# Kernel optimization log

Hardware: AMD Instinct MI355X
Metric: run time of the kernel (lower is better)

The kernel has to match this reference:

```python
import jax, jax.numpy as jnp
import numpy as np

CLAMP_MAX = float(np.log(100.0))  # temperature clamp from MoELayer


def setup_inputs() -> dict:
    key = jax.random.key(0)
    ks = jax.random.split(key, 4)
    N, D, H, E = 524288, 128, 512, 8
    x = jax.random.normal(ks[0], (N, D), dtype=jnp.float32)
    # per-expert MLP params, stacked along expert axis; scaled like torch Linear init
    W1 = jax.random.normal(ks[1], (E, D, H), dtype=jnp.float32) / np.sqrt(D)
    b1 = jnp.zeros((E, H), dtype=jnp.float32)
    W2 = jax.random.normal(ks[2], (E, H, D), dtype=jnp.float32) / np.sqrt(H)
    b2 = jnp.zeros((E, D), dtype=jnp.float32)
    temperature = jnp.full((1,), np.log(2.0), dtype=jnp.float32)  # init from MoELayer
    return {"x": x, "W1": W1, "b1": b1, "W2": W2, "b2": b2,
            "temperature": temperature}


def reference(x, W1, b1, W2, b2, temperature):
    # Pretraining proportional router: tokens split into E contiguous equal
    # chunks (route_prob == 1), so dispatch/combine is a reshape.
    E = W1.shape[0]
    N, D = x.shape
    xe = x.reshape(E, N // E, D)                      # [E, n, D] dispatched tokens
    h = jax.nn.relu(jnp.einsum('end,edh->enh', xe, W1) + b1[:, None, :])
    y = jnp.einsum('enh,ehd->end', h, W2) + b2[:, None, :]
    logit_scale = jnp.exp(jnp.minimum(temperature, CLAMP_MAX))  # scalar [1]
    out = y.reshape(N, D) * logit_scale
    return out
```

## Files before the change

kernel.cpp:

```cpp
#include <hip/hip_runtime.h>


#define CLAMP_MAXV 4.605170185988091f

typedef __attribute__((ext_vector_type(8))) short s16x8;
typedef __attribute__((ext_vector_type(4))) float f32x4;
typedef __attribute__((ext_vector_type(4))) unsigned short u16x4;
typedef __attribute__((ext_vector_type(8))) unsigned short u16x8;

static __device__ __forceinline__ unsigned short f2bf(float f) {
  union { float f; unsigned int u; } v; v.f = f;
  unsigned int r = v.u + 0x7FFFu + ((v.u >> 16) & 1u);
  return (unsigned short)(r >> 16);
}

static __device__ __forceinline__ void gll16(const void* src, void* dst) {
  __builtin_amdgcn_global_load_lds((const __attribute__((address_space(1))) void*)src,
                                   (__attribute__((address_space(3))) void*)dst, 16, 0, 0);
}

#define LBAR() do { \
  asm volatile("s_waitcnt lgkmcnt(0)" ::: "memory"); \
  __builtin_amdgcn_s_barrier(); \
  __builtin_amdgcn_sched_barrier(0); \
} while (0)

__global__ void conv_w(const float* __restrict__ W1, const float* __restrict__ W2,
                       unsigned short* __restrict__ w1t, unsigned short* __restrict__ w2t) {
  int idx = blockIdx.x * 256 + threadIdx.x;
  if (idx < 65536) {
    int h  = idx & 511;
    int d0 = ((idx >> 9) & 15) << 3;
    int e  = idx >> 13;
    const float* src = W1 + ((size_t)e << 16);
    u16x8 v;
#pragma unroll
    for (int j = 0; j < 8; ++j) v[j] = f2bf(src[(size_t)(d0 + j) * 512 + h]);
    *(u16x8*)(w1t + ((((size_t)e << 9) + h) << 7) + d0) = v;
  } else {
    int i2 = idx - 65536;
    int d  = i2 & 127;
    int h0 = ((i2 >> 7) & 63) << 3;
    int e  = i2 >> 13;
    const float* src = W2 + ((size_t)e << 16);
    u16x8 v;
#pragma unroll
    for (int j = 0; j < 8; ++j) v[j] = f2bf(src[(size_t)(h0 + j) * 128 + d]);
    *(u16x8*)(w2t + ((((size_t)e << 7) + d) << 9) + h0) = v;
  }
}

__global__ __launch_bounds__(1024, 4) void moe_fused(
    const float* __restrict__ x,
    const float* __restrict__ b1,
    const float* __restrict__ b2,
    const float* __restrict__ temp,
    const unsigned short* __restrict__ w1t,
    const unsigned short* __restrict__ w2t,
    float* __restrict__ out)
{
  __shared__ __align__(16) char smem[133120];
  char* const w1s  = smem;
  char* const hsb0 = smem + 98304;
  char* const hsb1 = smem + 106496;
  char* const xs   = smem + 114688;
  float* const b1s = (float*)(smem + 131072);

  const int tid  = threadIdx.x;
  const int lane = tid & 63;
  const int wid  = tid >> 6;
  const int l15  = lane & 15;
  const int lg   = lane >> 4;
  const int blk  = blockIdx.x;
  const int e    = blk >> 6;
  const size_t tok0 = (size_t)blk << 10;

  const unsigned short* w1g = w1t + ((size_t)e << 16);
  const unsigned short* w2g = w2t + ((size_t)e << 16);
  const float* xblk = x + (tok0 << 7);
  float* const oblk = out + (tok0 << 7);

#pragma unroll
  for (int k = 0; k < 6; ++k) {
    int s = tid + (k << 10);
    int hl = s >> 4, sr = s & 15;
    gll16(w1g + ((size_t)(hl + 128) << 7) + ((sr ^ (hl & 7)) << 3), w1s + (s << 4));
  }

  if (tid < 512) b1s[tid] = b1[(e << 9) + tid];

  f32x4 xv[2];
  xv[0] = *(const f32x4*)(xblk + (tid << 3));
  xv[1] = *(const f32x4*)(xblk + (tid << 3) + 4);

  const int xtok = tid >> 4;
  const unsigned xaddr = (unsigned)((xtok << 8) + ((tid & 15) << 4)) ^ (unsigned)((xtok & 7) << 4);

  if (wid < 8) {
    const int hr  = wid & 3;
    const int tq0 = (wid >> 2) << 5;
    const unsigned hl2 = (unsigned)(((hr << 4) + (lg << 2)) << 1);

    s16x8 w1r[2][4];
#pragma unroll
    for (int c = 0; c < 2; ++c) {
      const int hrow = (c << 6) + (hr << 4) + l15;
#pragma unroll
      for (int ks = 0; ks < 4; ++ks)
        w1r[c][ks] = *(const s16x8*)(w1g + ((size_t)hrow << 7) + (ks << 5) + (lg << 3));
    }

    __syncthreads();

#pragma unroll 1
    for (int t = 0; t < 16; ++t) {
      u16x8 p;
#pragma unroll
      for (int i = 0; i < 8; ++i) p[i] = f2bf(xv[i >> 2][i & 3]);
      *(u16x8*)(xs + xaddr) = p;
      LBAR();

      s16x8 xb[2][4];
#pragma unroll
      for (int j = 0; j < 2; ++j) {
        int tk = tq0 + (j << 4) + l15;
#pragma unroll
        for (int ks = 0; ks < 4; ++ks) {
          unsigned koff = (unsigned)((ks << 6) + (lg << 4));
          xb[j][ks] = *(const s16x8*)(xs + (((unsigned)(tk << 8) + koff) ^ (unsigned)((tk & 7) << 4)));
        }
      }

#pragma unroll
      for (int c = 0; c <= 8; ++c) {
        if (c < 8) {
          f32x4 bias = *(const f32x4*)(b1s + (c << 6) + (hr << 4) + (lg << 2));
          f32x4 acc1[2];
          acc1[0] = (f32x4){0.f, 0.f, 0.f, 0.f};
          acc1[1] = (f32x4){0.f, 0.f, 0.f, 0.f};
          if (c < 2) {
#pragma unroll
            for (int j = 0; j < 2; ++j)
#pragma unroll
              for (int ks = 0; ks < 4; ++ks)
                acc1[j] = __builtin_amdgcn_mfma_f32_16x16x32_bf16(w1r[c][ks], xb[j][ks], acc1[j], 0, 0, 0);
          } else {
            const int hrow = (c << 6) + (hr << 4) + l15;
            const unsigned hswz = (unsigned)((hrow & 7) << 4);
            s16x8 a[4];
#pragma unroll
            for (int ks = 0; ks < 4; ++ks) {
              unsigned koff = (unsigned)((ks << 6) + (lg << 4));
              a[ks] = *(const s16x8*)(w1s + (((unsigned)((hrow - 128) << 8) + koff) ^ hswz));
            }
#pragma unroll
            for (int j = 0; j < 2; ++j)
#pragma unroll
              for (int ks = 0; ks < 4; ++ks)
                acc1[j] = __builtin_amdgcn_mfma_f32_16x16x32_bf16(a[ks], xb[j][ks], acc1[j], 0, 0, 0);
          }

          char* const hw = (c & 1) ? hsb1 : hsb0;
#pragma unroll
          for (int j = 0; j < 2; ++j) {
            int tk = tq0 + (j << 4) + l15;
            u16x4 qv;
#pragma unroll
            for (int r = 0; r < 4; ++r)
              qv[r] = f2bf(fmaxf(acc1[j][r] + bias[r], 0.f));
            *(u16x4*)(hw + (((unsigned)(tk << 7) + hl2) ^ (unsigned)((tk & 7) << 4))) = qv;
          }
        }
        if (c == 4 && t < 15) {
          const float* xn = xblk + (((size_t)t + 1) << 13);
          xv[0] = *(const f32x4*)(xn + (tid << 3));
          xv[1] = *(const f32x4*)(xn + (tid << 3) + 4);
        }
        LBAR();
      }
    }
  } else {
    const int cw = wid - 8;
    const int dlane = (cw << 4) + l15;

    s16x8 w2f[8][2];
#pragma unroll
    for (int c = 0; c < 8; ++c)
#pragma unroll
      for (int ks = 0; ks < 2; ++ks)
        w2f[c][ks] = *(const s16x8*)(w2g + ((size_t)dlane << 9) + (c << 6) + (ks << 5) + (lg << 3));

    const float b2v   = b2[(e << 7) + dlane];
    const float scale = expf(fminf(temp[0], CLAMP_MAXV));

    __syncthreads();

#pragma unroll 1
    for (int t = 0; t < 16; ++t) {
      u16x8 p;
#pragma unroll
      for (int i = 0; i < 8; ++i) p[i] = f2bf(xv[i >> 2][i & 3]);
      *(u16x8*)(xs + xaddr) = p;
      LBAR();

      f32x4 acc2[4];
#pragma unroll
      for (int i = 0; i < 4; ++i) acc2[i] = (f32x4){0.f, 0.f, 0.f, 0.f};

#pragma unroll
      for (int c = 0; c <= 8; ++c) {
        if (c >= 1) {
          const int cc = c - 1;
          char* const hrd = (cc & 1) ? hsb1 : hsb0;
#pragma unroll
          for (int ii = 0; ii < 4; ++ii) {
            int tk = (ii << 4) + l15;
            unsigned tswz = (unsigned)((tk & 7) << 4);
#pragma unroll
            for (int ks = 0; ks < 2; ++ks) {
              unsigned koff = (unsigned)((ks << 6) + (lg << 4));
              s16x8 ha = *(const s16x8*)(hrd + (((unsigned)(tk << 7) + koff) ^ tswz));
              acc2[ii] = __builtin_amdgcn_mfma_f32_16x16x32_bf16(ha, w2f[cc][ks], acc2[ii], 0, 0, 0);
            }
          }
        }
        if (c == 4 && t < 15) {
          const float* xn = xblk + (((size_t)t + 1) << 13);
          xv[0] = *(const f32x4*)(xn + (tid << 3));
          xv[1] = *(const f32x4*)(xn + (tid << 3) + 4);
        }
        LBAR();
      }

      float* og = oblk + ((size_t)t << 13);
#pragma unroll
      for (int i = 0; i < 4; ++i) {
#pragma unroll
        for (int r = 0; r < 4; ++r) {
          int tk = (i << 4) + (lg << 2) + r;
          og[((size_t)tk << 7) + dlane] = (acc2[i][r] + b2v) * scale;
        }
      }
    }
  }
}

__global__ void moe_naive(const float* __restrict__ x, const float* __restrict__ W1,
                          const float* __restrict__ b1, const float* __restrict__ W2,
                          const float* __restrict__ b2, const float* __restrict__ temp,
                          float* __restrict__ out) {
  __shared__ float xr[128];
  __shared__ float hrow[512];
  int t = blockIdx.x;
  int e = t >> 16;
  int tx = threadIdx.x;
  xr[tx] = x[((size_t)t << 7) + tx];
  __syncthreads();
  const float* w1e = W1 + ((size_t)e << 16);
  for (int h = tx; h < 512; h += 128) {
    float s = b1[(e << 9) + h];
    for (int d = 0; d < 128; ++d) s += xr[d] * w1e[(size_t)d * 512 + h];
    hrow[h] = fmaxf(s, 0.f);
  }
  __syncthreads();
  const float* w2e = W2 + ((size_t)e << 16);
  float s = b2[(e << 7) + tx];
  for (int h = 0; h < 512; ++h) s += hrow[h] * w2e[(size_t)h * 128 + tx];
  out[((size_t)t << 7) + tx] = s * expf(fminf(temp[0], CLAMP_MAXV));
}

extern "C" void kernel_launch(void* const* d_in, const int* in_sizes, int n_in,
                              void* d_out, int out_size, void* d_ws, size_t ws_size,
                              hipStream_t stream) {
  const float* x    = (const float*)d_in[0];
  const float* W1   = (const float*)d_in[1];
  const float* b1   = (const float*)d_in[2];
  const float* W2   = (const float*)d_in[3];
  const float* b2   = (const float*)d_in[4];
  const float* temp = (const float*)d_in[5];
  float* out = (float*)d_out;

  const size_t WS_NEEDED = 2u * 524288u * sizeof(unsigned short);
  if (ws_size >= WS_NEEDED) {
    unsigned short* w1t = (unsigned short*)d_ws;
    unsigned short* w2t = w1t + 524288;
    conv_w<<<512, 256, 0, stream>>>(W1, W2, w1t, w2t);
    moe_fused<<<512, 1024, 0, stream>>>(x, b1, b2, temp, w1t, w2t, out);
  } else {
    moe_naive<<<524288, 128, 0, stream>>>(x, W1, b1, W2, b2, temp, out);
  }
}
```

Measured before the change: 178.6 us.

## Software-pipeline MoE stages across token tiles to drop per-tile barriers

Restructures the warp-specialized loop so the final W2 chunk of each tile and its output store run in the first step of the next tile. This removes the extra ninth barrier step per tile. The x tile conversion to bf16 and the xb register reloads are moved inside the chunk loop, hiding them behind MFMA work instead of paying for them in a separate barrier phase. It also moves one W1 chunk from registers into LDS (7 chunks in shared memory, 1 in registers), which raises shared memory per block to about 146 KB and frees VGPRs.

```diff
diff --git a/kernel.cpp b/kernel.cpp
--- a/kernel.cpp
+++ b/kernel.cpp
@@ -59,12 +59,12 @@
     const unsigned short* __restrict__ w2t,
     float* __restrict__ out)
 {
-  __shared__ __align__(16) char smem[133120];
+  __shared__ __align__(16) char smem[149504];
   char* const w1s  = smem;
-  char* const hsb0 = smem + 98304;
-  char* const hsb1 = smem + 106496;
-  char* const xs   = smem + 114688;
-  float* const b1s = (float*)(smem + 131072);
+  char* const hsb0 = smem + 114688;
+  char* const hsb1 = smem + 122880;
+  char* const xs   = smem + 131072;
+  float* const b1s = (float*)(smem + 147456);
 
   const int tid  = threadIdx.x;
   const int lane = tid & 63;
@@ -81,12 +81,11 @@
   float* const oblk = out + (tok0 << 7);
 
 #pragma unroll
-  for (int k = 0; k < 6; ++k) {
+  for (int k = 0; k < 7; ++k) {
     int s = tid + (k << 10);
     int hl = s >> 4, sr = s & 15;
-    gll16(w1g + ((size_t)(hl + 128) << 7) + ((sr ^ (hl & 7)) << 3), w1s + (s << 4));
-  }
-
+    gll16(w1g + ((size_t)(hl + 64) << 7) + ((sr ^ (hl & 7)) << 3), w1s + (s << 4));
+  }
   if (tid < 512) b1s[tid] = b1[(e << 9) + tid];
 
   f32x4 xv[2];
@@ -101,81 +100,95 @@
     const int tq0 = (wid >> 2) << 5;
     const unsigned hl2 = (unsigned)(((hr << 4) + (lg << 2)) << 1);
 
-    s16x8 w1r[2][4];
-#pragma unroll
-    for (int c = 0; c < 2; ++c) {
-      const int hrow = (c << 6) + (hr << 4) + l15;
+    s16x8 w1r[4];
+    {
+      const int hrow = (hr << 4) + l15;
 #pragma unroll
       for (int ks = 0; ks < 4; ++ks)
-        w1r[c][ks] = *(const s16x8*)(w1g + ((size_t)hrow << 7) + (ks << 5) + (lg << 3));
+        w1r[ks] = *(const s16x8*)(w1g + ((size_t)hrow << 7) + (ks << 5) + (lg << 3));
     }
 
     __syncthreads();
+
+    {
+      u16x8 p;
+#pragma unroll
+      for (int i = 0; i < 8; ++i) p[i] = f2bf(xv[i >> 2][i & 3]);
+      *(u16x8*)(xs + xaddr) = p;
+    }
+    LBAR();
+
+    s16x8 xb[2][4];
+#pragma unroll
+    for (int j = 0; j < 2; ++j) {
+      int tk = tq0 + (j << 4) + l15;
+#pragma unroll
+      for (int ks = 0; ks < 4; ++ks) {
+        unsigned koff = (unsigned)((ks << 6) + (lg << 4));
+        xb[j][ks] = *(const s16x8*)(xs + (((unsigned)(tk << 8) + koff) ^ (unsigned)((tk & 7) << 4)));
+      }
+    }
 
 #pragma unroll 1
     for (int t = 0; t < 16; ++t) {
-      u16x8 p;
-#pragma unroll
-      for (int i = 0; i < 8; ++i) p[i] = f2bf(xv[i >> 2][i & 3]);
-      *(u16x8*)(xs + xaddr) = p;
-      LBAR();
-
-      s16x8 xb[2][4];
-#pragma unroll
-      for (int j = 0; j < 2; ++j) {
-        int tk = tq0 + (j << 4) + l15;
-#pragma unroll
-        for (int ks = 0; ks < 4; ++ks) {
-          unsigned koff = (unsigned)((ks << 6) + (lg << 4));
-          xb[j][ks] = *(const s16x8*)(xs + (((unsigned)(tk << 8) + koff) ^ (unsigned)((tk & 7) << 4)));
-        }
-      }
-
-#pragma unroll
-      for (int c = 0; c <= 8; ++c) {
-        if (c < 8) {
-          f32x4 bias = *(const f32x4*)(b1s + (c << 6) + (hr << 4) + (lg << 2));
-          f32x4 acc1[2];
-          acc1[0] = (f32x4){0.f, 0.f, 0.f, 0.f};
-          acc1[1] = (f32x4){0.f, 0.f, 0.f, 0.f};
-          if (c < 2) {
-#pragma unroll
-            for (int j = 0; j < 2; ++j)
-#pragma unroll
-              for (int ks = 0; ks < 4; ++ks)
-                acc1[j] = __builtin_amdgcn_mfma_f32_16x16x32_bf16(w1r[c][ks], xb[j][ks], acc1[j], 0, 0, 0);
-          } else {
-            const int hrow = (c << 6) + (hr << 4) + l15;
-            const unsigned hswz = (unsigned)((hrow & 7) << 4);
-            s16x8 a[4];
-#pragma unroll
-            for (int ks = 0; ks < 4; ++ks) {
-              unsigned koff = (unsigned)((ks << 6) + (lg << 4));
-              a[ks] = *(const s16x8*)(w1s + (((unsigned)((hrow - 128) << 8) + koff) ^ hswz));
-            }
-#pragma unroll
-            for (int j = 0; j < 2; ++j)
-#pragma unroll
-              for (int ks = 0; ks < 4; ++ks)
-                acc1[j] = __builtin_amdgcn_mfma_f32_16x16x32_bf16(a[ks], xb[j][ks], acc1[j], 0, 0, 0);
+#pragma unroll
+      for (int c = 0; c < 8; ++c) {
+        s16x8 a[4];
+        if (c == 0) {
+#pragma unroll
+          for (int ks = 0; ks < 4; ++ks) a[ks] = w1r[ks];
+        } else {
+          const int hl = (c << 6) - 64 + (hr << 4) + l15;
+          const unsigned hswz = (unsigned)((hl & 7) << 4);
+#pragma unroll
+          for (int ks = 0; ks < 4; ++ks) {
+            unsigned koff = (unsigned)((ks << 6) + (lg << 4));
+            a[ks] = *(const s16x8*)(w1s + (((unsigned)(hl << 8) + koff) ^ hswz));
           }
-
-          char* const hw = (c & 1) ? hsb1 : hsb0;
-#pragma unroll
-          for (int j = 0; j < 2; ++j) {
-            int tk = tq0 + (j << 4) + l15;
-            u16x4 qv;
-#pragma unroll
-            for (int r = 0; r < 4; ++r)
-              qv[r] = f2bf(fmaxf(acc1[j][r] + bias[r], 0.f));
-            *(u16x4*)(hw + (((unsigned)(tk << 7) + hl2) ^ (unsigned)((tk & 7) << 4))) = qv;
-          }
-        }
+        }
+        f32x4 bias = *(const f32x4*)(b1s + (c << 6) + (hr << 4) + (lg << 2));
+        f32x4 acc1[2];
+        acc1[0] = (f32x4){0.f, 0.f, 0.f, 0.f};
+        acc1[1] = (f32x4){0.f, 0.f, 0.f, 0.f};
+#pragma unroll
+        for (int j = 0; j < 2; ++j)
+#pragma unroll
+          for (int ks = 0; ks < 4; ++ks)
+            acc1[j] = __builtin_amdgcn_mfma_f32_16x16x32_bf16(a[ks], xb[j][ks], acc1[j], 0, 0, 0);
+
+        char* const hw = (c & 1) ? hsb1 : hsb0;
+#pragma unroll
+        for (int j = 0; j < 2; ++j) {
+          int tk = tq0 + (j << 4) + l15;
+          u16x4 qv;
+#pragma unroll
+          for (int r = 0; r < 4; ++r)
+            qv[r] = f2bf(fmaxf(acc1[j][r] + bias[r], 0.f));
+          *(u16x4*)(hw + (((unsigned)(tk << 7) + hl2) ^ (unsigned)((tk & 7) << 4))) = qv;
+        }
+
         if (c == 4 && t < 15) {
           const float* xn = xblk + (((size_t)t + 1) << 13);
           xv[0] = *(const f32x4*)(xn + (tid << 3));
           xv[1] = *(const f32x4*)(xn + (tid << 3) + 4);
         }
+        if (c == 5 && t < 15) {
+          u16x8 p;
+#pragma unroll
+          for (int i = 0; i < 8; ++i) p[i] = f2bf(xv[i >> 2][i & 3]);
+          *(u16x8*)(xs + xaddr) = p;
+        }
+        if (c == 7 && t < 15) {
+#pragma unroll
+          for (int j = 0; j < 2; ++j) {
+            int tk = tq0 + (j << 4) + l15;
+#pragma unroll
+            for (int ks = 0; ks < 4; ++ks) {
+              unsigned koff = (unsigned)((ks << 6) + (lg << 4));
+              xb[j][ks] = *(const s16x8*)(xs + (((unsigned)(tk << 8) + koff) ^ (unsigned)((tk & 7) << 4)));
+            }
+          }
+        }
         LBAR();
       }
     }
@@ -195,21 +208,48 @@
 
     __syncthreads();
 
+    {
+      u16x8 p;
+#pragma unroll
+      for (int i = 0; i < 8; ++i) p[i] = f2bf(xv[i >> 2][i & 3]);
+      *(u16x8*)(xs + xaddr) = p;
+    }
+    LBAR();
+
+    f32x4 acc2[4];
+#pragma unroll
+    for (int i = 0; i < 4; ++i) acc2[i] = (f32x4){0.f, 0.f, 0.f, 0.f};
+
 #pragma unroll 1
     for (int t = 0; t < 16; ++t) {
-      u16x8 p;
-#pragma unroll
-      for (int i = 0; i < 8; ++i) p[i] = f2bf(xv[i >> 2][i & 3]);
-      *(u16x8*)(xs + xaddr) = p;
-      LBAR();
-
-      f32x4 acc2[4];
-#pragma unroll
-      for (int i = 0; i < 4; ++i) acc2[i] = (f32x4){0.f, 0.f, 0.f, 0.f};
-
-#pragma unroll
-      for (int c = 0; c <= 8; ++c) {
-        if (c >= 1) {
+#pragma unroll
+      for (int c = 0; c < 8; ++c) {
+        if (c == 0) {
+          if (t > 0) {
+#pragma unroll
+            for (int ii = 0; ii < 4; ++ii) {
+              int tk = (ii << 4) + l15;
+              unsigned tswz = (unsigned)((tk & 7) << 4);
+#pragma unroll
+              for (int ks = 0; ks < 2; ++ks) {
+                unsigned koff = (unsigned)((ks << 6) + (lg << 4));
+                s16x8 ha = *(const s16x8*)(hsb1 + (((unsigned)(tk << 7) + koff) ^ tswz));
+                acc2[ii] = __builtin_amdgcn_mfma_f32_16x16x32_bf16(ha, w2f[7][ks], acc2[ii], 0, 0, 0);
+              }
+            }
+            float* og = oblk + ((size_t)(t - 1) << 13);
+#pragma unroll
+            for (int ii = 0; ii < 4; ++ii) {
+#pragma unroll
+              for (int r = 0; r < 4; ++r) {
+                int tk = (ii << 4) + (lg << 2) + r;
+                og[((size_t)tk << 7) + dlane] = (acc2[ii][r] + b2v) * scale;
+              }
+            }
+          }
+#pragma unroll
+          for (int i = 0; i < 4; ++i) acc2[i] = (f32x4){0.f, 0.f, 0.f, 0.f};
+        } else {
           const int cc = c - 1;
           char* const hrd = (cc & 1) ? hsb1 : hsb0;
 #pragma unroll
@@ -224,22 +264,40 @@
             }
           }
         }
+
         if (c == 4 && t < 15) {
           const float* xn = xblk + (((size_t)t + 1) << 13);
           xv[0] = *(const f32x4*)(xn + (tid << 3));
           xv[1] = *(const f32x4*)(xn + (tid << 3) + 4);
         }
+        if (c == 5 && t < 15) {
+          u16x8 p;
+#pragma unroll
+          for (int i = 0; i < 8; ++i) p[i] = f2bf(xv[i >> 2][i & 3]);
+          *(u16x8*)(xs + xaddr) = p;
+        }
         LBAR();
       }
-
-      float* og = oblk + ((size_t)t << 13);
-#pragma unroll
-      for (int i = 0; i < 4; ++i) {
-#pragma unroll
-        for (int r = 0; r < 4; ++r) {
-          int tk = (i << 4) + (lg << 2) + r;
-          og[((size_t)tk << 7) + dlane] = (acc2[i][r] + b2v) * scale;
-        }
+    }
+
+#pragma unroll
+    for (int ii = 0; ii < 4; ++ii) {
+      int tk = (ii << 4) + l15;
+      unsigned tswz = (unsigned)((tk & 7) << 4);
+#pragma unroll
+      for (int ks = 0; ks < 2; ++ks) {
+        unsigned koff = (unsigned)((ks << 6) + (lg << 4));
+        s16x8 ha = *(const s16x8*)(hsb1 + (((unsigned)(tk << 7) + koff) ^ tswz));
+        acc2[ii] = __builtin_amdgcn_mfma_f32_16x16x32_bf16(ha, w2f[7][ks], acc2[ii], 0, 0, 0);
+      }
+    }
+    float* og = oblk + ((size_t)15 << 13);
+#pragma unroll
+    for (int ii = 0; ii < 4; ++ii) {
+#pragma unroll
+      for (int r = 0; r < 4; ++r) {
+        int tk = (ii << 4) + (lg << 2) + r;
+        og[((size_t)tk << 7) + dlane] = (acc2[ii][r] + b2v) * scale;
       }
     }
   }
```

Measured after the change: 185.1 us. 3.7% more time.
